# Optimization experiments

Hardware: AMD Instinct MI355X
Metric: run time of the kernel (lower is better)

The kernel has to match this reference:

```python
import jax, jax.numpy as jnp
import numpy as np

N_BINS = 15


def setup_inputs() -> dict:
    key = jax.random.key(0)
    k1, k2 = jax.random.split(key)
    N, C = 4000000, 64
    logits = jax.random.normal(k1, (N, C), dtype=jnp.float32)
    labels = jax.random.randint(k2, (N,), 0, C, dtype=jnp.int64)
    temperature = jnp.ones((1,), dtype=jnp.float32)
    return {"logits": logits, "labels": labels, "temperature": temperature}


def reference(logits, labels, temperature):
    # softmax over classes at given temperature (onevsrest=False path)
    probs = jax.nn.softmax(logits / temperature, axis=1)
    confidences = jnp.max(probs, axis=1)          # [N]
    predictions = jnp.argmax(probs, axis=1)       # [N]
    accuracies = (predictions == labels).astype(confidences.dtype)

    # bin i covers (i/n_bins, (i+1)/n_bins]; conf >= 1/C > 0 so ceil-1 maps correctly
    bin_idx = jnp.clip(
        jnp.ceil(confidences * N_BINS).astype(jnp.int32) - 1, 0, N_BINS - 1)

    count = jax.ops.segment_sum(jnp.ones_like(confidences), bin_idx, num_segments=N_BINS)
    conf_sum = jax.ops.segment_sum(confidences, bin_idx, num_segments=N_BINS)
    acc_sum = jax.ops.segment_sum(accuracies, bin_idx, num_segments=N_BINS)

    nonempty = count > 0
    safe_count = jnp.where(nonempty, count, 1.0)
    gap = jnp.abs(conf_sum / safe_count - acc_sum / safe_count)  # [n_bins]
    prop = count / confidences.shape[0]

    ece = jnp.sum(jnp.where(nonempty, gap * prop, 0.0))
    mce = jnp.max(jnp.where(nonempty, gap, 0.0))
    return ece, mce
```

## Files before the change

### kernel.cpp

```cpp
#include <hip/hip_runtime.h>

#define NBINS 15

typedef float f32x4 __attribute__((ext_vector_type(4)));

__global__ __launch_bounds__(256) void ece_partial(
    const f32x4* __restrict__ logits4,
    const int*   __restrict__ labels,
    const float* __restrict__ temperature,
    float*       __restrict__ gbins,
    int N)
{
    __shared__ float sbins[3 * NBINS];
    const int tid = threadIdx.x;
    if (tid < 3 * NBINS) sbins[tid] = 0.0f;
    __syncthreads();

    const float invT = 1.0f / temperature[0];

    const int lane = tid & 63;
    const int wIn  = tid >> 6;
    const long long gWave = (long long)blockIdx.x * 4 + wIn;
    const long long nWave = (long long)gridDim.x * 4;
    const long long step  = nWave * 16;

    const int sub = lane & 3;
    const int rIw = lane >> 2;

    long long r0 = gWave * 16;
    if (r0 < (long long)N) {
        long long row   = r0 + rIw;
        bool     cvalid = row < (long long)N;
        long long crc   = cvalid ? row : (long long)(N - 1);

        const f32x4* p = logits4 + crc * 16 + sub;
        f32x4 c0 = __builtin_nontemporal_load(p);
        f32x4 c1 = __builtin_nontemporal_load(p + 4);
        f32x4 c2 = __builtin_nontemporal_load(p + 8);
        f32x4 c3 = __builtin_nontemporal_load(p + 12);
        int   clbl = labels[crc];

        for (;;) {
            const long long nr0 = r0 + step;
            const bool have_next = nr0 < (long long)N;

            f32x4 n0, n1, n2, n3; int nlbl = 0; bool nvalid = false;
            if (have_next) {
                const long long nrow = nr0 + rIw;
                nvalid = nrow < (long long)N;
                const long long nrc = nvalid ? nrow : (long long)(N - 1);
                const f32x4* np = logits4 + nrc * 16 + sub;
                n0 = __builtin_nontemporal_load(np);
                n1 = __builtin_nontemporal_load(np + 4);
                n2 = __builtin_nontemporal_load(np + 8);
                n3 = __builtin_nontemporal_load(np + 12);
                nlbl = labels[nrc];
            }

            float s;
            {
                const float a0 = __expf(c0.x * invT), a1 = __expf(c0.y * invT);
                const float a2 = __expf(c0.z * invT), a3 = __expf(c0.w * invT);
                const float b0 = __expf(c1.x * invT), b1 = __expf(c1.y * invT);
                const float b2 = __expf(c1.z * invT), b3 = __expf(c1.w * invT);
                const float e0 = __expf(c2.x * invT), e1 = __expf(c2.y * invT);
                const float e2 = __expf(c2.z * invT), e3 = __expf(c2.w * invT);
                const float d0 = __expf(c3.x * invT), d1 = __expf(c3.y * invT);
                const float d2 = __expf(c3.z * invT), d3 = __expf(c3.w * invT);
                s = (((a0 + a1) + (a2 + a3)) + ((b0 + b1) + (b2 + b3)))
                  + (((e0 + e1) + (e2 + e3)) + ((d0 + d1) + (d2 + d3)));
            }

            float m = fmaxf(fmaxf(fmaxf(c0.x, c0.y), fmaxf(c0.z, c0.w)),
                            fmaxf(fmaxf(c1.x, c1.y), fmaxf(c1.z, c1.w)));
            m = fmaxf(m, fmaxf(fmaxf(fmaxf(c2.x, c2.y), fmaxf(c2.z, c2.w)),
                               fmaxf(fmaxf(c3.x, c3.y), fmaxf(c3.z, c3.w))));

            s += __shfl_xor(s, 1);
            s += __shfl_xor(s, 2);
            m = fmaxf(m, __shfl_xor(m, 1));
            m = fmaxf(m, __shfl_xor(m, 2));

            const float conf = __expf(m * invT) * __builtin_amdgcn_rcpf(s);
            int bin = (int)ceilf(conf * (float)NBINS) - 1;
            bin = bin < 0 ? 0 : (bin > NBINS - 1 ? NBINS - 1 : bin);

            if (cvalid) {
                if (sub == 0) {
                    atomicAdd(&sbins[bin],         1.0f);
                    atomicAdd(&sbins[NBINS + bin], conf);
                }
                if (((clbl >> 2) & 3) == sub) {
                    const int k = clbl >> 4;
                    const int j = clbl & 3;
                    const f32x4 vk = (k < 2) ? ((k & 1) ? c1 : c0)
                                             : ((k & 1) ? c3 : c2);
                    const float vl = (j < 2) ? ((j & 1) ? vk.y : vk.x)
                                             : ((j & 1) ? vk.w : vk.z);
                    if (vl == m) atomicAdd(&sbins[2 * NBINS + bin], 1.0f);
                }
            }

            if (!have_next) break;
            c0 = n0; c1 = n1; c2 = n2; c3 = n3;
            clbl = nlbl; cvalid = nvalid;
            r0 = nr0;
        }
    }

    __syncthreads();
    if (tid < 3 * NBINS) {
        const float v = sbins[tid];
        if (v != 0.0f) atomicAdd(&gbins[tid], v);
    }
}

__global__ void ece_finalize(const float* __restrict__ gbins,
                             float* __restrict__ out, float invN)
{
    if (threadIdx.x == 0 && blockIdx.x == 0) {
        float ece = 0.0f, mce = 0.0f;
        #pragma unroll
        for (int i = 0; i < NBINS; ++i) {
            const float c  = gbins[i];
            const float cs = gbins[NBINS + i];
            const float as = gbins[2 * NBINS + i];
            if (c > 0.0f) {
                const float gap = fabsf(cs / c - as / c);
                ece += gap * (c * invN);
                mce = fmaxf(mce, gap);
            }
        }
        out[0] = ece;
        out[1] = mce;
    }
}

extern "C" void kernel_launch(void* const* d_in, const int* in_sizes, int n_in,
                              void* d_out, int out_size, void* d_ws, size_t ws_size,
                              hipStream_t stream) {
    const f32x4* logits4     = (const f32x4*)d_in[0];
    const int*   labels      = (const int*)d_in[1];
    const float* temperature = (const float*)d_in[2];
    float*       out         = (float*)d_out;
    float*       gbins       = (float*)d_ws;

    const int N = in_sizes[1];

    hipMemsetAsync(gbins, 0, 3 * NBINS * sizeof(float), stream);

    const int block = 256;
    const int grid  = 2048;
    ece_partial<<<grid, block, 0, stream>>>(logits4, labels, temperature, gbins, N);
    ece_finalize<<<1, 64, 0, stream>>>(gbins, out, 1.0f / (float)N);
}
```

Baseline: 184.9 us.

## Fuse finalize into histogram kernel via last-block ticket and privatize LDS bins

Drops the separate finalize kernel: each block increments a global ticket after a threadfence, and the last block to arrive reads the global bins through atomics and writes ECE and MCE. This removes one kernel launch and its gap. The shared-memory histogram is also replicated 16 ways, one copy per row slot within a wave, to cut LDS atomic contention, with a 16-way reduction before the global atomics. The cost is a small extra zeroing pass and reduction per block, plus reliance on the memory fence for correctness.

```diff
diff --git a/kernel.cpp b/kernel.cpp
--- a/kernel.cpp
+++ b/kernel.cpp
@@ -4,16 +4,19 @@
 
 typedef float f32x4 __attribute__((ext_vector_type(4)));
 
-__global__ __launch_bounds__(256) void ece_partial(
+__global__ __launch_bounds__(256) void ece_fused(
     const f32x4* __restrict__ logits4,
     const int*   __restrict__ labels,
     const float* __restrict__ temperature,
     float*       __restrict__ gbins,
-    int N)
+    int*         __restrict__ ticket,
+    float*       __restrict__ out,
+    int N, int nblocks)
 {
-    __shared__ float sbins[3 * NBINS];
+    __shared__ float sbins[16][3 * NBINS];
     const int tid = threadIdx.x;
-    if (tid < 3 * NBINS) sbins[tid] = 0.0f;
+    for (int i = tid; i < 16 * 3 * NBINS; i += 256)
+        (&sbins[0][0])[i] = 0.0f;
     __syncthreads();
 
     const float invT = 1.0f / temperature[0];
@@ -87,8 +90,8 @@
 
             if (cvalid) {
                 if (sub == 0) {
-                    atomicAdd(&sbins[bin],         1.0f);
-                    atomicAdd(&sbins[NBINS + bin], conf);
+                    atomicAdd(&sbins[rIw][bin],         1.0f);
+                    atomicAdd(&sbins[rIw][NBINS + bin], conf);
                 }
                 if (((clbl >> 2) & 3) == sub) {
                     const int k = clbl >> 4;
@@ -97,7 +100,7 @@
                                              : ((k & 1) ? c3 : c2);
                     const float vl = (j < 2) ? ((j & 1) ? vk.y : vk.x)
                                              : ((j & 1) ? vk.w : vk.z);
-                    if (vl == m) atomicAdd(&sbins[2 * NBINS + bin], 1.0f);
+                    if (vl == m) atomicAdd(&sbins[rIw][2 * NBINS + bin], 1.0f);
                 }
             }
 
@@ -110,29 +113,32 @@
 
     __syncthreads();
     if (tid < 3 * NBINS) {
-        const float v = sbins[tid];
+        float v = 0.0f;
+        #pragma unroll
+        for (int r = 0; r < 16; ++r) v += sbins[r][tid];
         if (v != 0.0f) atomicAdd(&gbins[tid], v);
     }
-}
 
-__global__ void ece_finalize(const float* __restrict__ gbins,
-                             float* __restrict__ out, float invN)
-{
-    if (threadIdx.x == 0 && blockIdx.x == 0) {
-        float ece = 0.0f, mce = 0.0f;
-        #pragma unroll
-        for (int i = 0; i < NBINS; ++i) {
-            const float c  = gbins[i];
-            const float cs = gbins[NBINS + i];
-            const float as = gbins[2 * NBINS + i];
-            if (c > 0.0f) {
-                const float gap = fabsf(cs / c - as / c);
-                ece += gap * (c * invN);
-                mce = fmaxf(mce, gap);
+    __threadfence();
+    if (tid == 0) {
+        const int t = atomicAdd(ticket, 1);
+        if (t == nblocks - 1) {
+            const float invN = 1.0f / (float)N;
+            float ece = 0.0f, mce = 0.0f;
+            #pragma unroll
+            for (int i = 0; i < NBINS; ++i) {
+                const float c  = atomicAdd(&gbins[i],             0.0f);
+                const float cs = atomicAdd(&gbins[NBINS + i],     0.0f);
+                const float as = atomicAdd(&gbins[2 * NBINS + i], 0.0f);
+                if (c > 0.0f) {
+                    const float gap = fabsf(cs / c - as / c);
+                    ece += gap * (c * invN);
+                    mce = fmaxf(mce, gap);
+                }
             }
+            out[0] = ece;
+            out[1] = mce;
         }
-        out[0] = ece;
-        out[1] = mce;
     }
 }
 
@@ -144,13 +150,14 @@
     const float* temperature = (const float*)d_in[2];
     float*       out         = (float*)d_out;
     float*       gbins       = (float*)d_ws;
+    int*         ticket      = (int*)d_ws + 48;
 
     const int N = in_sizes[1];
 
-    hipMemsetAsync(gbins, 0, 3 * NBINS * sizeof(float), stream);
+    hipMemsetAsync(d_ws, 0, 64 * sizeof(float), stream);
 
     const int block = 256;
     const int grid  = 2048;
-    ece_partial<<<grid, block, 0, stream>>>(logits4, labels, temperature, gbins, N);
-    ece_finalize<<<1, 64, 0, stream>>>(gbins, out, 1.0f / (float)N);
+    ece_fused<<<grid, block, 0, stream>>>(logits4, labels, temperature,
+                                          gbins, ticket, out, N, grid);
 }
```

Result: slower. 579.2 us (+213.3%).
